# Optimization experiments

Hardware: AMD Instinct MI355X
Metric: run time of the kernel (lower is better)

The kernel has to match this reference:

```python
import jax, jax.numpy as jnp
import numpy as np


def setup_inputs() -> dict:
    key = jax.random.key(0)
    k1, k2, k3, k4 = jax.random.split(key, 4)
    B, S, d_in, d_out = 4, 2048, 1024, 1024
    x = jax.random.normal(k1, (B, S, d_in), dtype=jnp.float32)
    # torch nn.Linear weight is [d_out, d_in]; we store transposed [d_in, d_out]
    Wq = jax.random.normal(k2, (d_in, d_out), dtype=jnp.float32) * (1.0 / np.sqrt(d_in))
    Wk = jax.random.normal(k3, (d_in, d_out), dtype=jnp.float32) * (1.0 / np.sqrt(d_in))
    Wv = jax.random.normal(k4, (d_in, d_out), dtype=jnp.float32) * (1.0 / np.sqrt(d_in))
    return {"x": x, "Wq": Wq, "Wk": Wk, "Wv": Wv}


def reference(x, Wq, Wk, Wv):
    # x: [B, S, d_in]
    B, S, d_in = x.shape
    q = jnp.einsum("bsd,de->bse", x, Wq)
    k = jnp.einsum("bsd,de->bse", x, Wk)
    v = jnp.einsum("bsd,de->bse", x, Wv)
    scores = jnp.einsum("bqe,bke->bqk", q, k)  # [B, S, S]
    causal = jnp.triu(jnp.ones((S, S), dtype=bool), k=1)  # True above diagonal
    scores = jnp.where(causal[None, :, :], -jnp.inf, scores)
    # NOTE: original scales by sqrt(d_in), not sqrt(d_out)
    scale = jnp.asarray(1.0 / np.sqrt(d_in), dtype=scores.dtype)
    weights = jax.nn.softmax(scores * scale, axis=-1)
    # dropout p=0.0 -> identity
    return jnp.einsum("bqk,bke->bqe", weights, v)
```

## Files before the change

kernel.cpp:

```cpp
#include <hip/hip_runtime.h>
#include <hip/hip_bf16.h>

typedef __attribute__((ext_vector_type(8))) short short8;
typedef __attribute__((ext_vector_type(4))) float f32x4;
typedef unsigned short ushort_t;

__device__ __forceinline__ ushort_t f2bf(float f) {
    union { __hip_bfloat16 h; ushort_t u; } c;
    c.h = __float2bfloat16(f);
    return c.u;
}

__device__ __forceinline__ void gload16(const ushort_t* g, ushort_t* l) {
    __builtin_amdgcn_global_load_lds(
        (const __attribute__((address_space(1))) void*)g,
        (__attribute__((address_space(3))) void*)l, 16, 0, 0);
}

__global__ __launch_bounds__(256) void k_convert_x(const float* __restrict__ x,
                                                   ushort_t* __restrict__ xb) {
    size_t idx = ((size_t)blockIdx.x * 256 + threadIdx.x) * 8;
    float4 a = *(const float4*)(x + idx);
    float4 b = *(const float4*)(x + idx + 4);
    short8 o;
    o[0] = (short)f2bf(a.x); o[1] = (short)f2bf(a.y);
    o[2] = (short)f2bf(a.z); o[3] = (short)f2bf(a.w);
    o[4] = (short)f2bf(b.x); o[5] = (short)f2bf(b.y);
    o[6] = (short)f2bf(b.z); o[7] = (short)f2bf(b.w);
    *(short8*)(xb + idx) = o;
}

__global__ __launch_bounds__(256) void k_transpose_w(const float* __restrict__ W0,
                                                     const float* __restrict__ W1,
                                                     const float* __restrict__ W2,
                                                     ushort_t* __restrict__ Wt) {
    const float* W = (blockIdx.z == 0) ? W0 : (blockIdx.z == 1) ? W1 : W2;
    ushort_t* out = Wt + (size_t)blockIdx.z * 1024 * 1024;
    __shared__ float tile[32][33];
    int tx = threadIdx.x, ty = threadIdx.y;
    int d0 = blockIdx.y * 32, e0 = blockIdx.x * 32;
#pragma unroll
    for (int i = 0; i < 32; i += 8)
        tile[ty + i][tx] = W[(size_t)(d0 + ty + i) * 1024 + e0 + tx];
    __syncthreads();
#pragma unroll
    for (int i = 0; i < 32; i += 8)
        out[(size_t)(e0 + ty + i) * 1024 + d0 + tx] = f2bf(tile[tx][ty + i]);
}

__global__ __launch_bounds__(256) void k_transpose_v(const ushort_t* __restrict__ V,
                                                     ushort_t* __restrict__ Vt) {
    int b = blockIdx.z;
    const ushort_t* in = V + (size_t)b * 2048 * 1024;
    ushort_t* out = Vt + (size_t)b * 1024 * 2048;
    __shared__ ushort_t tile[32][33];
    int tx = threadIdx.x, ty = threadIdx.y;
    int e0 = blockIdx.x * 32, j0 = blockIdx.y * 32;
#pragma unroll
    for (int i = 0; i < 32; i += 8)
        tile[ty + i][tx] = in[(size_t)(j0 + ty + i) * 1024 + e0 + tx];
    __syncthreads();
#pragma unroll
    for (int i = 0; i < 32; i += 8)
        out[(size_t)(e0 + ty + i) * 2048 + j0 + tx] = tile[tx][ty + i];
}

template <int MODE>
__global__ __launch_bounds__(256) void k_gemm(const ushort_t* __restrict__ Abase,
                                              const ushort_t* __restrict__ Bbase,
                                              void* __restrict__ Cbase) {
    const int bm = blockIdx.x, bn = blockIdx.y, bz = blockIdx.z;

    const ushort_t* A;
    const ushort_t* B;
    int lda, ldb, nk;
    if constexpr (MODE == 0) {
        A = Abase; lda = 1024;
        B = Bbase + (size_t)bz * 1024 * 1024; ldb = 1024;
        nk = 32;
    } else if constexpr (MODE == 1) {
        if (bn > bm) return;
        A = Abase + (size_t)bz * 2048 * 1024; lda = 1024;
        B = Bbase + (size_t)bz * 2048 * 1024; ldb = 1024;
        nk = 32;
    } else {
        A = Abase + (size_t)bz * 2048 * 4096; lda = 4096;
        B = Bbase + (size_t)bz * 1024 * 2048; ldb = 2048;
        nk = (bm + 1) * 4;
    }

    __shared__ ushort_t As[128 * 32];
    __shared__ ushort_t Bs[128 * 32];

    const int tid = threadIdx.x;
    const int l = tid & 63, wid = tid >> 6;
    const int wr = (wid >> 1) * 64, wc = (wid & 1) * 64;
    const int lr = l & 15, kc = (l >> 4) * 8;

    const int srow = tid >> 2, skb = (tid & 3) * 8;
    const ushort_t* ag = A + (size_t)(bm * 128 + srow) * lda + skb;
    const ushort_t* bg = B + (size_t)(bn * 128 + srow) * ldb + skb;
    const size_t a64 = (size_t)64 * lda, b64 = (size_t)64 * ldb;
    ushort_t* al = As + tid * 8;
    ushort_t* bl = Bs + tid * 8;

    f32x4 zero = {0.f, 0.f, 0.f, 0.f};
    f32x4 acc[4][4];
#pragma unroll
    for (int m = 0; m < 4; ++m)
#pragma unroll
        for (int n = 0; n < 4; ++n) acc[m][n] = zero;

    for (int ks = 0; ks < nk; ++ks) {
        __syncthreads();
        gload16(ag, al);
        gload16(ag + a64, al + 2048);
        gload16(bg, bl);
        gload16(bg + b64, bl + 2048);
        ag += 32; bg += 32;
        __syncthreads();

        short8 a[4], b[4];
#pragma unroll
        for (int m = 0; m < 4; ++m)
            a[m] = *(const short8*)&As[(wr + m * 16 + lr) * 32 + kc];
#pragma unroll
        for (int n = 0; n < 4; ++n)
            b[n] = *(const short8*)&Bs[(wc + n * 16 + lr) * 32 + kc];
#pragma unroll
        for (int m = 0; m < 4; ++m)
#pragma unroll
            for (int n = 0; n < 4; ++n)
                acc[m][n] = __builtin_amdgcn_mfma_f32_16x16x32_bf16(a[m], b[n], acc[m][n], 0, 0, 0);
    }

    const int rbase = (l >> 4) * 4;
    const int cbase = l & 15;
#pragma unroll
    for (int m = 0; m < 4; ++m) {
#pragma unroll
        for (int n = 0; n < 4; ++n) {
            int row0 = wr + m * 16 + rbase;
            int col = wc + n * 16 + cbase;
            int gcol = bn * 128 + col;
#pragma unroll
            for (int r = 0; r < 4; ++r) {
                int grow = bm * 128 + row0 + r;
                float v = acc[m][n][r];
                if constexpr (MODE == 0) {
                    ushort_t* C = (ushort_t*)Cbase + (size_t)bz * 8192 * 1024;
                    C[(size_t)grow * 1024 + gcol] = f2bf(v);
                } else if constexpr (MODE == 1) {
                    float* C = (float*)Cbase + (size_t)bz * 2048 * 2048;
                    if (gcol <= grow) C[(size_t)grow * 2048 + gcol] = v * 0.03125f;
                } else {
                    float* C = (float*)Cbase + (size_t)bz * 2048 * 1024;
                    C[(size_t)grow * 1024 + gcol] = v;
                }
            }
        }
    }
}

__global__ __launch_bounds__(256) void k_softmax(float* __restrict__ scores) {
    const int t = blockIdx.x;
    const int i = t & 2047;
    float* row = scores + (size_t)t * 2048;
    const int tid = threadIdx.x;
    const int j0 = tid * 8;

    float4 f0 = *(const float4*)(row + j0);
    float4 f1 = *(const float4*)(row + j0 + 4);
    float v[8] = {f0.x, f0.y, f0.z, f0.w, f1.x, f1.y, f1.z, f1.w};

    float m = -3.0e38f;
#pragma unroll
    for (int e = 0; e < 8; ++e)
        if (j0 + e <= i) m = fmaxf(m, v[e]);
#pragma unroll
    for (int off = 32; off > 0; off >>= 1) m = fmaxf(m, __shfl_down(m, off, 64));

    __shared__ float redm[4];
    __shared__ float reds[4];
    const int lane = tid & 63, wid = tid >> 6;
    if (lane == 0) redm[wid] = m;
    __syncthreads();
    m = fmaxf(fmaxf(redm[0], redm[1]), fmaxf(redm[2], redm[3]));

    float p[8];
    float s = 0.f;
#pragma unroll
    for (int e = 0; e < 8; ++e) {
        p[e] = (j0 + e <= i) ? __expf(v[e] - m) : 0.f;
        s += p[e];
    }
#pragma unroll
    for (int off = 32; off > 0; off >>= 1) s += __shfl_down(s, off, 64);
    if (lane == 0) reds[wid] = s;
    __syncthreads();
    s = reds[0] + reds[1] + reds[2] + reds[3];
    float inv = 1.f / s;

    short8 o;
#pragma unroll
    for (int e = 0; e < 8; ++e) o[e] = (short)f2bf(p[e] * inv);
    *(short8*)((ushort_t*)row + j0) = o;
}

extern "C" void kernel_launch(void* const* d_in, const int* in_sizes, int n_in,
                              void* d_out, int out_size, void* d_ws, size_t ws_size,
                              hipStream_t stream) {
    const float* x  = (const float*)d_in[0];
    const float* Wq = (const float*)d_in[1];
    const float* Wk = (const float*)d_in[2];
    const float* Wv = (const float*)d_in[3];

    char* ws = (char*)d_ws;
    ushort_t* xb     = (ushort_t*)(ws);
    ushort_t* Wt     = (ushort_t*)(ws + 16777216);
    ushort_t* QKV    = (ushort_t*)(ws + 23068672);
    ushort_t* Vt     = (ushort_t*)(ws + 73400320);
    float*    scores = (float*)   (ws + 90177536);

    ushort_t* Q = QKV;
    ushort_t* K = QKV + (size_t)8192 * 1024;
    ushort_t* V = QKV + (size_t)2 * 8192 * 1024;

    k_convert_x<<<4096, 256, 0, stream>>>(x, xb);
    k_transpose_w<<<dim3(32, 32, 3), dim3(32, 8), 0, stream>>>(Wq, Wk, Wv, Wt);
    k_gemm<0><<<dim3(64, 8, 3), 256, 0, stream>>>(xb, Wt, QKV);
    k_transpose_v<<<dim3(32, 64, 4), dim3(32, 8), 0, stream>>>(V, Vt);
    k_gemm<1><<<dim3(16, 16, 4), 256, 0, stream>>>(Q, K, scores);
    k_softmax<<<8192, 256, 0, stream>>>(scores);
    k_gemm<2><<<dim3(16, 8, 4), 256, 0, stream>>>((const ushort_t*)scores, Vt, (float*)d_out);
}
```

Measured before the change: 205.7 us.

## Replace QKV projection GEMM with 256x128 tile, double-buffered swizzled LDS pipeline

Swaps the generic 128x128 projection GEMM for a dedicated 512-thread kernel computing 256x128 tiles with a BK=64 step split into two halves. It double-buffers LDS with asynchronous global-to-LDS loads issued several stages ahead, paced by vmcnt waits and a single barrier per step. It also XOR-swizzles the LDS layout to reduce bank conflicts and raises wave priority around the MFMA block. The goal is to hide global load latency and cut synchronisation and LDS overhead in the largest GEMM, at the cost of more LDS and registers per block.

```diff
diff --git a/kernel.cpp b/kernel.cpp
--- a/kernel.cpp
+++ b/kernel.cpp
@@ -65,6 +65,88 @@
         out[(size_t)(e0 + ty + i) * 2048 + j0 + tx] = tile[tx][ty + i];
 }
 
+__global__ __launch_bounds__(512, 2) void k_proj256(const ushort_t* __restrict__ Abase,
+                                                    const ushort_t* __restrict__ Bbase,
+                                                    ushort_t* __restrict__ Cbase) {
+    const int bm = blockIdx.x, bn = blockIdx.y, bz = blockIdx.z;
+    const ushort_t* A = Abase;
+    const ushort_t* B = Bbase + (size_t)bz * 1048576;
+    constexpr int LDA = 1024, LDB = 1024, NT = 16;
+
+    __shared__ ushort_t Asm[2][2][8192];
+    __shared__ ushort_t Bsm[2][2][4096];
+
+    const int tid = threadIdx.x;
+    const int l = tid & 63, w = tid >> 6;
+    const int wrow = w >> 2, wcol = w & 3;
+    const int lr = l & 15, lg = l >> 4;
+    const int axoff = (lg * 8) ^ ((lr & 3) << 3);
+
+    const int srow = tid >> 2;
+    const int scol = ((tid & 3) * 8) ^ (((tid >> 2) & 3) << 3);
+    const ushort_t* Ag = A + (size_t)(bm * 256 + srow) * LDA + scol;
+    const ushort_t* Bg = B + (size_t)(bn * 128 + srow) * LDB + scol;
+
+    auto stage = [&](int s) {
+        if (s >= 4 * NT) return;
+        const int ts = s >> 2, j = s & 3, kh = j >> 1, db = ts & 1;
+        if (j & 1) {
+            gload16(Bg + ts * 64 + kh * 32, &Bsm[db][kh][tid * 8]);
+        } else {
+            const ushort_t* src = Ag + ts * 64 + kh * 32;
+            gload16(src, &Asm[db][kh][tid * 8]);
+            gload16(src + (size_t)128 * LDA, &Asm[db][kh][tid * 8 + 4096]);
+        }
+    };
+
+    f32x4 zero = {0.f, 0.f, 0.f, 0.f};
+    f32x4 acc[8][2];
+#pragma unroll
+    for (int m = 0; m < 8; ++m) { acc[m][0] = zero; acc[m][1] = zero; }
+
+    stage(0); stage(1); stage(2); stage(3); stage(4); stage(5);
+    asm volatile("s_waitcnt vmcnt(6)" ::: "memory");
+    __builtin_amdgcn_s_barrier();
+
+#pragma unroll 4
+    for (int p = 0; p < 2 * NT; ++p) {
+        const int kh = p & 1, db = (p >> 1) & 1;
+        short8 a[8], b[2];
+#pragma unroll
+        for (int m = 0; m < 8; ++m)
+            a[m] = *(const short8*)&Asm[db][kh][(wrow * 128 + m * 16 + lr) * 32 + axoff];
+#pragma unroll
+        for (int n = 0; n < 2; ++n)
+            b[n] = *(const short8*)&Bsm[db][kh][(wcol * 32 + n * 16 + lr) * 32 + axoff];
+        stage(2 * p + 6);
+        stage(2 * p + 7);
+        __builtin_amdgcn_s_setprio(1);
+#pragma unroll
+        for (int m = 0; m < 8; ++m)
+#pragma unroll
+            for (int n = 0; n < 2; ++n)
+                acc[m][n] = __builtin_amdgcn_mfma_f32_16x16x32_bf16(a[m], b[n], acc[m][n], 0, 0, 0);
+        __builtin_amdgcn_s_setprio(0);
+        asm volatile("s_waitcnt vmcnt(6)" ::: "memory");
+        __builtin_amdgcn_s_barrier();
+    }
+    asm volatile("s_waitcnt vmcnt(0)" ::: "memory");
+
+    ushort_t* C = Cbase + (size_t)bz * 8388608;
+    const int rb = lg * 4;
+#pragma unroll
+    for (int m = 0; m < 8; ++m)
+#pragma unroll
+        for (int n = 0; n < 2; ++n) {
+            int gcol = bn * 128 + wcol * 32 + n * 16 + lr;
+#pragma unroll
+            for (int r = 0; r < 4; ++r) {
+                int grow = bm * 256 + wrow * 128 + m * 16 + rb + r;
+                C[(size_t)grow * 1024 + gcol] = f2bf(acc[m][n][r]);
+            }
+        }
+}
+
 template <int MODE>
 __global__ __launch_bounds__(256) void k_gemm(const ushort_t* __restrict__ Abase,
                                               const ushort_t* __restrict__ Bbase,
@@ -74,11 +156,7 @@
     const ushort_t* A;
     const ushort_t* B;
     int lda, ldb, nk;
-    if constexpr (MODE == 0) {
-        A = Abase; lda = 1024;
-        B = Bbase + (size_t)bz * 1024 * 1024; ldb = 1024;
-        nk = 32;
-    } else if constexpr (MODE == 1) {
+    if constexpr (MODE == 1) {
         if (bn > bm) return;
         A = Abase + (size_t)bz * 2048 * 1024; lda = 1024;
         B = Bbase + (size_t)bz * 2048 * 1024; ldb = 1024;
@@ -147,10 +225,7 @@
             for (int r = 0; r < 4; ++r) {
                 int grow = bm * 128 + row0 + r;
                 float v = acc[m][n][r];
-                if constexpr (MODE == 0) {
-                    ushort_t* C = (ushort_t*)Cbase + (size_t)bz * 8192 * 1024;
-                    C[(size_t)grow * 1024 + gcol] = f2bf(v);
-                } else if constexpr (MODE == 1) {
+                if constexpr (MODE == 1) {
                     float* C = (float*)Cbase + (size_t)bz * 2048 * 2048;
                     if (gcol <= grow) C[(size_t)grow * 2048 + gcol] = v * 0.03125f;
                 } else {
@@ -228,7 +303,7 @@
 
     k_convert_x<<<4096, 256, 0, stream>>>(x, xb);
     k_transpose_w<<<dim3(32, 32, 3), dim3(32, 8), 0, stream>>>(Wq, Wk, Wv, Wt);
-    k_gemm<0><<<dim3(64, 8, 3), 256, 0, stream>>>(xb, Wt, QKV);
+    k_proj256<<<dim3(32, 8, 3), 512, 0, stream>>>(xb, Wt, QKV);
     k_transpose_v<<<dim3(32, 64, 4), dim3(32, 8), 0, stream>>>(V, Vt);
     k_gemm<1><<<dim3(16, 16, 4), 256, 0, stream>>>(Q, K, scores);
     k_softmax<<<8192, 256, 0, stream>>>(scores);
```

Result: slower. 215.3 us (+4.7%).

## Fuse softmax into score and PV GEMMs with deferred row normalization

Applied to the files above, without the earlier changes.

Removes the separate softmax kernel. The QK^T GEMM now writes bf16 exp(score*scale) directly without max subtraction. The PV GEMM computes row sums with an extra MFMA against a ones vector and divides at the end. It also launches only the 136 lower-triangular tiles instead of early-returning, and interleaves row blocks in the PV GEMM to balance causal work. Skipping max subtraction risks overflow for large scores, and the sum is taken from bf16-rounded values.

```diff
diff --git a/kernel.cpp b/kernel.cpp
--- a/kernel.cpp
+++ b/kernel.cpp
@@ -69,22 +69,30 @@
 __global__ __launch_bounds__(256) void k_gemm(const ushort_t* __restrict__ Abase,
                                               const ushort_t* __restrict__ Bbase,
                                               void* __restrict__ Cbase) {
-    const int bm = blockIdx.x, bn = blockIdx.y, bz = blockIdx.z;
-
+    const int bz = blockIdx.z;
+    int bm, bn;
     const ushort_t* A;
     const ushort_t* B;
     int lda, ldb, nk;
     if constexpr (MODE == 0) {
+        bm = blockIdx.x; bn = blockIdx.y;
         A = Abase; lda = 1024;
         B = Bbase + (size_t)bz * 1024 * 1024; ldb = 1024;
         nk = 32;
     } else if constexpr (MODE == 1) {
-        if (bn > bm) return;
+        int x = blockIdx.x;
+        bm = (int)((sqrtf(8.f * x + 1.f) - 1.f) * 0.5f);
+        while ((bm + 1) * (bm + 2) / 2 <= x) ++bm;
+        while (bm * (bm + 1) / 2 > x) --bm;
+        bn = x - bm * (bm + 1) / 2;
         A = Abase + (size_t)bz * 2048 * 1024; lda = 1024;
         B = Bbase + (size_t)bz * 2048 * 1024; ldb = 1024;
         nk = 32;
     } else {
-        A = Abase + (size_t)bz * 2048 * 4096; lda = 4096;
+        int xr = blockIdx.x;
+        bm = (xr & 1) ? (15 - (xr >> 1)) : (xr >> 1);
+        bn = blockIdx.y;
+        A = Abase + (size_t)bz * 2048 * 2048; lda = 2048;
         B = Bbase + (size_t)bz * 1024 * 2048; ldb = 2048;
         nk = (bm + 1) * 4;
     }
@@ -110,6 +118,13 @@
     for (int m = 0; m < 4; ++m)
 #pragma unroll
         for (int n = 0; n < 4; ++n) acc[m][n] = zero;
+
+    f32x4 rs[4];
+    short8 ones;
+#pragma unroll
+    for (int e = 0; e < 8; ++e) ones[e] = (short)0x3F80;
+#pragma unroll
+    for (int m = 0; m < 4; ++m) rs[m] = zero;
 
     for (int ks = 0; ks < nk; ++ks) {
         __syncthreads();
@@ -132,10 +147,24 @@
 #pragma unroll
             for (int n = 0; n < 4; ++n)
                 acc[m][n] = __builtin_amdgcn_mfma_f32_16x16x32_bf16(a[m], b[n], acc[m][n], 0, 0, 0);
+        if constexpr (MODE == 2) {
+#pragma unroll
+            for (int m = 0; m < 4; ++m)
+                rs[m] = __builtin_amdgcn_mfma_f32_16x16x32_bf16(a[m], ones, rs[m], 0, 0, 0);
+        }
     }
 
     const int rbase = (l >> 4) * 4;
     const int cbase = l & 15;
+
+    float inv[4][4];
+    if constexpr (MODE == 2) {
+#pragma unroll
+        for (int m = 0; m < 4; ++m)
+#pragma unroll
+            for (int r = 0; r < 4; ++r) inv[m][r] = 1.0f / rs[m][r];
+    }
+
 #pragma unroll
     for (int m = 0; m < 4; ++m) {
 #pragma unroll
@@ -151,60 +180,17 @@
                     ushort_t* C = (ushort_t*)Cbase + (size_t)bz * 8192 * 1024;
                     C[(size_t)grow * 1024 + gcol] = f2bf(v);
                 } else if constexpr (MODE == 1) {
-                    float* C = (float*)Cbase + (size_t)bz * 2048 * 2048;
-                    if (gcol <= grow) C[(size_t)grow * 2048 + gcol] = v * 0.03125f;
+                    ushort_t* C = (ushort_t*)Cbase + (size_t)bz * 2048 * 2048;
+                    ushort_t pv = (gcol <= grow) ? f2bf(__expf(v * 0.03125f))
+                                                 : (ushort_t)0;
+                    C[(size_t)grow * 2048 + gcol] = pv;
                 } else {
                     float* C = (float*)Cbase + (size_t)bz * 2048 * 1024;
-                    C[(size_t)grow * 1024 + gcol] = v;
+                    C[(size_t)grow * 1024 + gcol] = v * inv[m][r];
                 }
             }
         }
     }
-}
-
-__global__ __launch_bounds__(256) void k_softmax(float* __restrict__ scores) {
-    const int t = blockIdx.x;
-    const int i = t & 2047;
-    float* row = scores + (size_t)t * 2048;
-    const int tid = threadIdx.x;
-    const int j0 = tid * 8;
-
-    float4 f0 = *(const float4*)(row + j0);
-    float4 f1 = *(const float4*)(row + j0 + 4);
-    float v[8] = {f0.x, f0.y, f0.z, f0.w, f1.x, f1.y, f1.z, f1.w};
-
-    float m = -3.0e38f;
-#pragma unroll
-    for (int e = 0; e < 8; ++e)
-        if (j0 + e <= i) m = fmaxf(m, v[e]);
-#pragma unroll
-    for (int off = 32; off > 0; off >>= 1) m = fmaxf(m, __shfl_down(m, off, 64));
-
-    __shared__ float redm[4];
-    __shared__ float reds[4];
-    const int lane = tid & 63, wid = tid >> 6;
-    if (lane == 0) redm[wid] = m;
-    __syncthreads();
-    m = fmaxf(fmaxf(redm[0], redm[1]), fmaxf(redm[2], redm[3]));
-
-    float p[8];
-    float s = 0.f;
-#pragma unroll
-    for (int e = 0; e < 8; ++e) {
-        p[e] = (j0 + e <= i) ? __expf(v[e] - m) : 0.f;
-        s += p[e];
-    }
-#pragma unroll
-    for (int off = 32; off > 0; off >>= 1) s += __shfl_down(s, off, 64);
-    if (lane == 0) reds[wid] = s;
-    __syncthreads();
-    s = reds[0] + reds[1] + reds[2] + reds[3];
-    float inv = 1.f / s;
-
-    short8 o;
-#pragma unroll
-    for (int e = 0; e < 8; ++e) o[e] = (short)f2bf(p[e] * inv);
-    *(short8*)((ushort_t*)row + j0) = o;
 }
 
 extern "C" void kernel_launch(void* const* d_in, const int* in_sizes, int n_in,
@@ -220,7 +206,7 @@
     ushort_t* Wt     = (ushort_t*)(ws + 16777216);
     ushort_t* QKV    = (ushort_t*)(ws + 23068672);
     ushort_t* Vt     = (ushort_t*)(ws + 73400320);
-    float*    scores = (float*)   (ws + 90177536);
+    ushort_t* P      = (ushort_t*)(ws + 90177536);
 
     ushort_t* Q = QKV;
     ushort_t* K = QKV + (size_t)8192 * 1024;
@@ -230,7 +216,6 @@
     k_transpose_w<<<dim3(32, 32, 3), dim3(32, 8), 0, stream>>>(Wq, Wk, Wv, Wt);
     k_gemm<0><<<dim3(64, 8, 3), 256, 0, stream>>>(xb, Wt, QKV);
     k_transpose_v<<<dim3(32, 64, 4), dim3(32, 8), 0, stream>>>(V, Vt);
-    k_gemm<1><<<dim3(16, 16, 4), 256, 0, stream>>>(Q, K, scores);
-    k_softmax<<<8192, 256, 0, stream>>>(scores);
-    k_gemm<2><<<dim3(16, 8, 4), 256, 0, stream>>>((const ushort_t*)scores, Vt, (float*)d_out);
-}
+    k_gemm<1><<<dim3(136, 1, 4), 256, 0, stream>>>(Q, K, P);
+    k_gemm<2><<<dim3(16, 8, 4), 256, 0, stream>>>(P, Vt, (float*)d_out);
+}
```

After: 181.2 us. 11.9% less time.
